# Optimization experiments

Measured on AMD Instinct MI355X. Metric: run time of the kernel, lower is better.

The kernel has to match this reference:

```python
import jax, jax.numpy as jnp
import numpy as np

ANCHORS = np.array([[10.0, 13.0], [16.0, 30.0], [33.0, 23.0]], dtype=np.float32)
NUM_ANCHORS = 3
NUM_CLASSES = 80
OBJ_SCALE = 1.0
NOOBJ_SCALE = 100.0
EPS = 1e-12


def setup_inputs() -> dict:
    key = jax.random.key(0)
    ks = jax.random.split(key, 10)
    B, A, G, C = 32, NUM_ANCHORS, 52, NUM_CLASSES
    x = jax.random.normal(ks[0], (B, A * (C + 5), G, G), dtype=jnp.float32)
    tx = jax.random.uniform(ks[1], (B, A, G, G), dtype=jnp.float32)
    ty = jax.random.uniform(ks[2], (B, A, G, G), dtype=jnp.float32)
    tw = jax.random.normal(ks[3], (B, A, G, G), dtype=jnp.float32)
    th = jax.random.normal(ks[4], (B, A, G, G), dtype=jnp.float32)
    tconf = jax.random.uniform(ks[5], (B, A, G, G), dtype=jnp.float32)
    tcls = jax.random.uniform(ks[6], (B, A, G, G, C), dtype=jnp.float32)
    sum_weights1 = jax.random.uniform(ks[7], (B, A, G, G), dtype=jnp.float32)
    obj_mask = jax.random.randint(ks[8], (B, A, G, G), 0, 2).astype(bool)
    noobj_mask = jax.random.randint(ks[9], (B, A, G, G), 0, 2).astype(bool)
    return {"x": x, "tx": tx, "ty": ty, "tw": tw, "th": th, "tconf": tconf,
            "tcls": tcls, "sum_weights1": sum_weights1, "obj_mask": obj_mask,
            "noobj_mask": noobj_mask, "img_dim": 416}


def _bce(p, t):
    # torch BCELoss(reduction='none') on already-sigmoided probs
    return -(t * jnp.log(jnp.clip(p, EPS, 1.0)) + (1.0 - t) * jnp.log(jnp.clip(1.0 - p, EPS, 1.0)))


def reference(x, tx, ty, tw, th, tconf, tcls, sum_weights1, obj_mask, noobj_mask, img_dim):
    B, _, G, _ = x.shape
    A, C = NUM_ANCHORS, NUM_CLASSES
    stride = img_dim / G  # python float
    # [B, A, G, G, C+5]
    pred = x.reshape(B, A, C + 5, G, G).transpose(0, 1, 3, 4, 2)
    px = jax.nn.sigmoid(pred[..., 0])
    py = jax.nn.sigmoid(pred[..., 1])
    pw = pred[..., 2]
    ph = pred[..., 3]
    pred_conf = jax.nn.sigmoid(pred[..., 4])
    pred_cls = jax.nn.sigmoid(pred[..., 5:])

    grid_x = jnp.arange(G, dtype=x.dtype).reshape(1, 1, 1, G)  # varies along last axis
    grid_y = jnp.arange(G, dtype=x.dtype).reshape(1, 1, G, 1)
    scaled_anchors = jnp.asarray(ANCHORS) / jnp.asarray(stride, x.dtype)
    anchor_w = scaled_anchors[:, 0].reshape(1, A, 1, 1)
    anchor_h = scaled_anchors[:, 1].reshape(1, A, 1, 1)

    sg = jax.lax.stop_gradient  # mimics .data in pred_boxes construction
    pred_boxes = jnp.stack([
        sg(px) + jnp.broadcast_to(grid_x, px.shape),
        sg(py) + jnp.broadcast_to(grid_y, py.shape),
        jnp.exp(sg(pw)) * jnp.broadcast_to(anchor_w, pw.shape),
        jnp.exp(sg(ph)) * jnp.broadcast_to(anchor_h, ph.shape),
    ], axis=-1)  # [B, A, G, G, 4]

    output = jnp.concatenate([
        pred_boxes.reshape(B, -1, 4) * stride,
        pred_conf.reshape(B, -1, 1),
        pred_cls.reshape(B, -1, C),
    ], axis=-1)

    om = obj_mask.astype(x.dtype)
    nm = noobj_mask.astype(x.dtype)
    n_obj = jnp.maximum(om.sum(), 1.0)
    n_noobj = jnp.maximum(nm.sum(), 1.0)

    def wmse(p, t):
        # mean over obj elements of mse * sum_weights1
        return jnp.sum(om * (p - t) ** 2 * sum_weights1) / n_obj

    loss_x = wmse(px, tx)
    loss_y = wmse(py, ty)
    loss_w = wmse(pw, tw)
    loss_h = wmse(ph, th)

    bce_conf = _bce(pred_conf, tconf)
    loss_conf_obj = jnp.sum(om * bce_conf * sum_weights1) / n_obj
    loss_conf_noobj = jnp.sum(nm * bce_conf) / n_noobj
    loss_conf = OBJ_SCALE * loss_conf_obj + NOOBJ_SCALE * loss_conf_noobj

    # tcls[obj_mask] yields [N, C]; mean is over N*C
    loss_cls = jnp.sum(om[..., None] * _bce(pred_cls, tcls)) / (n_obj * C)

    total_loss = loss_x + loss_y + loss_w + loss_h + loss_conf + loss_cls
    return output, total_loss
```

## Files before the change

kernel.cpp:

```cpp
#include <hip/hip_runtime.h>

#define NB 32
#define NA 3
#define GD 52
#define GG 2704
#define NC 80
#define CHN 85
#define CPW 8
#define WPP 338
#define NPLANE (NB * NA)
#define NWAVE (NPLANE * WPP)
#define WPB 4
#define NBLK (NWAVE / WPB)
#define NXQ 170
#define NTQ 160
#define LXW 680
#define AUXW 80
#define RBLK 32

__device__ __forceinline__ float sigm_u(float u) { return __builtin_amdgcn_rcpf(u); }

__global__ __launch_bounds__(256) void yolo_main(
    const float* __restrict__ x,
    const float* __restrict__ tx, const float* __restrict__ ty,
    const float* __restrict__ tw, const float* __restrict__ th,
    const float* __restrict__ tconf, const float* __restrict__ tcls,
    const float* __restrict__ sw1,
    const int* __restrict__ om, const int* __restrict__ nm,
    const int* __restrict__ imgdim,
    float* __restrict__ out,
    float4* __restrict__ partials,
    double* __restrict__ accD)
{
    __shared__ float lx_all[WPB * LXW];
    __shared__ float la_all[WPB * AUXW];

    const int tid  = threadIdx.x;
    const int widx = tid >> 6, lane = tid & 63;
    const int wid  = blockIdx.x * WPB + widx;
    const int plane = wid / WPP;
    const int sblk  = wid - plane * WPP;
    const int a = plane % NA, b = plane / NA;
    const int s0 = sblk * CPW;
    float* lx = lx_all + widx * LXW;
    float* la = la_all + widx * AUXW;

    int iv = imgdim[0];
    float imgf = (iv > 0 && iv < 65536) ? (float)iv : __int_as_float(iv);
    const float stride = imgf / (float)GD;
    const float aw = (a == 0) ? 10.0f : ((a == 1) ? 16.0f : 33.0f);
    const float ah = (a == 0) ? 13.0f : ((a == 1) ? 30.0f : 23.0f);

    const long pbase = (long)plane * GG + s0;
    const float* xb = x + ((long)b * (NA * CHN) + a * CHN) * GG + s0;
    const float* tb = tcls + pbase * NC;

    float v0 = 0.0f, v1 = 0.0f;
    if (lane < CPW) {
        float vtx = tx[pbase + lane],    vty = ty[pbase + lane];
        float vtw = tw[pbase + lane],    vth = th[pbase + lane];
        float vtc = tconf[pbase + lane], vsw = sw1[pbase + lane];
        float vom = (float)om[pbase + lane], vnm = (float)nm[pbase + lane];
        int gcell = s0 + lane;
        int gyi = gcell / GD;
        la[0 * CPW + lane] = vtx;  la[1 * CPW + lane] = vty;
        la[2 * CPW + lane] = vtw;  la[3 * CPW + lane] = vth;
        la[4 * CPW + lane] = vtc;  la[5 * CPW + lane] = vom * vsw;
        la[6 * CPW + lane] = vnm;  la[7 * CPW + lane] = vom;
        la[8 * CPW + lane] = (float)(gcell - gyi * GD);
        la[9 * CPW + lane] = (float)gyi;
        v0 = vom; v1 = vnm;
    }

    float4 xr[3];
    #pragma unroll
    for (int k = 0; k < 3; ++k) {
        int q = lane + 64 * k;
        if (q < NXQ) {
            int ch = q >> 1, sq = (q & 1) << 2;
            xr[k] = *(const float4*)(xb + (long)ch * GG + sq);
        }
    }
    __builtin_amdgcn_wave_barrier();

    float4 tr[3]; float gk[3];
    #pragma unroll
    for (int k = 0; k < 3; ++k) {
        gk[k] = 0.0f;
        int q = lane + 64 * k;
        if (q < NTQ) {
            int s = q / 20, c4 = (q - s * 20) * 4;
            float g = la[7 * CPW + s];
            gk[k] = g;
            if (g != 0.0f) tr[k] = *(const float4*)(tb + s * NC + c4);
        }
    }

    float s_obj = 0.f, s_cn = 0.f, s_cl = 0.f;

    #pragma unroll
    for (int k = 0; k < 3; ++k) {
        int q = lane + 64 * k;
        if (q >= NXQ) continue;
        int ch = q >> 1, sq = (q & 1) << 2;
        float vv[4] = { xr[k].x, xr[k].y, xr[k].z, xr[k].w };
        if (ch >= 5) {
            #pragma unroll
            for (int j = 0; j < 4; ++j)
                lx[(sq + j) * CHN + ch] = sigm_u(1.0f + __expf(-vv[j]));
        } else if (ch == 0) {
            #pragma unroll
            for (int j = 0; j < 4; ++j) {
                int s = sq + j;
                float p = sigm_u(1.0f + __expf(-vv[j]));
                float d = p - la[0 * CPW + s];
                s_obj = fmaf(la[5 * CPW + s], d * d, s_obj);
                lx[s * CHN + 0] = (p + la[8 * CPW + s]) * stride;
            }
        } else if (ch == 1) {
            #pragma unroll
            for (int j = 0; j < 4; ++j) {
                int s = sq + j;
                float p = sigm_u(1.0f + __expf(-vv[j]));
                float d = p - la[1 * CPW + s];
                s_obj = fmaf(la[5 * CPW + s], d * d, s_obj);
                lx[s * CHN + 1] = (p + la[9 * CPW + s]) * stride;
            }
        } else if (ch == 2) {
            #pragma unroll
            for (int j = 0; j < 4; ++j) {
                int s = sq + j;
                float d = vv[j] - la[2 * CPW + s];
                s_obj = fmaf(la[5 * CPW + s], d * d, s_obj);
                lx[s * CHN + 2] = __expf(vv[j]) * aw;
            }
        } else if (ch == 3) {
            #pragma unroll
            for (int j = 0; j < 4; ++j) {
                int s = sq + j;
                float d = vv[j] - la[3 * CPW + s];
                s_obj = fmaf(la[5 * CPW + s], d * d, s_obj);
                lx[s * CHN + 3] = __expf(vv[j]) * ah;
            }
        } else {
            #pragma unroll
            for (int j = 0; j < 4; ++j) {
                int s = sq + j;
                float z = vv[j];
                float u = 1.0f + __expf(-z);
                float p = sigm_u(u);
                float t = la[4 * CPW + s];
                float bb = fmaf(1.0f - t, z, __logf(u));
                s_obj = fmaf(la[5 * CPW + s], bb, s_obj);
                s_cn  = fmaf(la[6 * CPW + s], bb, s_cn);
                lx[s * CHN + 4] = p;
            }
        }
    }
    __builtin_amdgcn_wave_barrier();

    float* ob = out + pbase * CHN;
    #pragma unroll
    for (int k = 0; k < 3; ++k) {
        int q = lane + 64 * k;
        if (q < NXQ) {
            float4 w4 = *(const float4*)&lx[4 * q];
            *(float4*)(ob + 4 * q) = w4;
        }
    }

    #pragma unroll
    for (int k = 0; k < 3; ++k) {
        if (gk[k] != 0.0f) {
            int q = lane + 64 * k;
            int s = q / 20, c4 = (q - s * 20) * 4;
            int base = s * CHN + 5 + c4;
            float tt[4] = { tr[k].x, tr[k].y, tr[k].z, tr[k].w };
            #pragma unroll
            for (int j = 0; j < 4; ++j) {
                float p = lx[base + j];
                s_cl -= fmaf(tt[j], __logf(p), (1.0f - tt[j]) * __logf(1.0f - p));
            }
        }
    }
    s_obj = fmaf(s_cl, 0.0125f, s_obj);

    float v2 = s_obj, v3 = s_cn;
    #pragma unroll
    for (int off = 32; off > 0; off >>= 1) {
        v0 += __shfl_down(v0, off, 64);
        v1 += __shfl_down(v1, off, 64);
        v2 += __shfl_down(v2, off, 64);
        v3 += __shfl_down(v3, off, 64);
    }
    if (lane == 0) {
        if (partials) {
            partials[wid] = make_float4(v0, v1, v2, v3);
        } else {
            atomicAdd(&accD[0], (double)v0);
            atomicAdd(&accD[8], (double)v1);
            atomicAdd(&accD[16], (double)v2);
            atomicAdd(&accD[24], (double)v3);
        }
    }
}

__global__ __launch_bounds__(256) void yolo_reduceA(const float4* __restrict__ partials,
                                                    float4* __restrict__ stage2)
{
    __shared__ float sred[4][4];
    const int tid = threadIdx.x, wv = tid >> 6, ln = tid & 63;
    float d0 = 0, d1 = 0, d2 = 0, d3 = 0;
    for (int i = blockIdx.x * 256 + tid; i < NWAVE; i += RBLK * 256) {
        float4 p = partials[i];
        d0 += p.x; d1 += p.y; d2 += p.z; d3 += p.w;
    }
    #pragma unroll
    for (int off = 32; off > 0; off >>= 1) {
        d0 += __shfl_down(d0, off, 64);
        d1 += __shfl_down(d1, off, 64);
        d2 += __shfl_down(d2, off, 64);
        d3 += __shfl_down(d3, off, 64);
    }
    if (ln == 0) { sred[wv][0] = d0; sred[wv][1] = d1; sred[wv][2] = d2; sred[wv][3] = d3; }
    __syncthreads();
    if (tid == 0)
        stage2[blockIdx.x] = make_float4(sred[0][0] + sred[1][0] + sred[2][0] + sred[3][0],
                                         sred[0][1] + sred[1][1] + sred[2][1] + sred[3][1],
                                         sred[0][2] + sred[1][2] + sred[2][2] + sred[3][2],
                                         sred[0][3] + sred[1][3] + sred[2][3] + sred[3][3]);
}

__global__ __launch_bounds__(64) void yolo_reduceB(const float4* __restrict__ stage2,
                                                   float* __restrict__ out_loss)
{
    const int ln = threadIdx.x;
    double d0 = 0, d1 = 0, d2 = 0, d3 = 0;
    if (ln < RBLK) {
        float4 p = stage2[ln];
        d0 = p.x; d1 = p.y; d2 = p.z; d3 = p.w;
    }
    #pragma unroll
    for (int off = 32; off > 0; off >>= 1) {
        d0 += __shfl_down(d0, off, 64);
        d1 += __shfl_down(d1, off, 64);
        d2 += __shfl_down(d2, off, 64);
        d3 += __shfl_down(d3, off, 64);
    }
    if (ln == 0) {
        double nobj = fmax(d0, 1.0), nnoobj = fmax(d1, 1.0);
        *out_loss = (float)(d2 / nobj + 100.0 * d3 / nnoobj);
    }
}

__global__ void yolo_final_atomic(const double* __restrict__ accD, float* __restrict__ out_loss)
{
    double nobj = fmax(accD[0], 1.0), nnoobj = fmax(accD[8], 1.0);
    *out_loss = (float)(accD[16] / nobj + 100.0 * accD[24] / nnoobj);
}

extern "C" void kernel_launch(void* const* d_in, const int* in_sizes, int n_in,
                              void* d_out, int out_size, void* d_ws, size_t ws_size,
                              hipStream_t stream)
{
    const float* x     = (const float*)d_in[0];
    const float* tx    = (const float*)d_in[1];
    const float* ty    = (const float*)d_in[2];
    const float* tw    = (const float*)d_in[3];
    const float* th    = (const float*)d_in[4];
    const float* tconf = (const float*)d_in[5];
    const float* tcls  = (const float*)d_in[6];
    const float* sw1   = (const float*)d_in[7];
    const int*   om    = (const int*)d_in[8];
    const int*   nm    = (const int*)d_in[9];
    const int*   img   = (const int*)d_in[10];
    float* out = (float*)d_out;

    const size_t need = (size_t)(NWAVE + RBLK) * sizeof(float4);
    dim3 grid(NBLK);

    if (ws_size >= need) {
        float4* partials = (float4*)d_ws;
        float4* stage2   = partials + NWAVE;
        yolo_main<<<grid, 256, 0, stream>>>(x, tx, ty, tw, th, tconf, tcls, sw1,
                                            om, nm, img, out, partials, nullptr);
        yolo_reduceA<<<RBLK, 256, 0, stream>>>(partials, stage2);
        yolo_reduceB<<<1, 64, 0, stream>>>(stage2, out + (out_size - 1));
    } else {
        double* accD = (double*)d_ws;
        hipMemsetAsync(d_ws, 0, 32 * sizeof(double), stream);
        yolo_main<<<grid, 256, 0, stream>>>(x, tx, ty, tw, th, tconf, tcls, sw1,
                                            om, nm, img, out, nullptr, accD);
        yolo_final_atomic<<<1, 1, 0, stream>>>(accD, out + (out_size - 1));
    }
}
```

Measured before the change: 57.67 us.

## Load per-cell targets into registers across the wave and shuffle the objectness mask

Every lane now loads the eight per-cell target values (indexed by lane&7) right after the x loads are issued, instead of lanes 0-7 loading them first. The objectness flag for the tcls gating comes from a width-8 shuffle rather than shared memory, so the gated tcls loads no longer wait behind an LDS write and barrier. The class BCE is also rewritten with log2 and a single fma per element, with the -ln2/80 scale folded into one constant. The cost is redundant scalar loads across 64 lanes and a slightly reshaped auxiliary LDS layout.

```diff
diff --git a/kernel.cpp b/kernel.cpp
--- a/kernel.cpp
+++ b/kernel.cpp
@@ -15,8 +15,9 @@
 #define NXQ 170
 #define NTQ 160
 #define LXW 680
-#define AUXW 80
+#define AUXW 72
 #define RBLK 32
+#define NEG_LN2_80 (-0.008664339757f)
 
 __device__ __forceinline__ float sigm_u(float u) { return __builtin_amdgcn_rcpf(u); }
 
@@ -55,23 +56,6 @@
     const float* xb = x + ((long)b * (NA * CHN) + a * CHN) * GG + s0;
     const float* tb = tcls + pbase * NC;
 
-    float v0 = 0.0f, v1 = 0.0f;
-    if (lane < CPW) {
-        float vtx = tx[pbase + lane],    vty = ty[pbase + lane];
-        float vtw = tw[pbase + lane],    vth = th[pbase + lane];
-        float vtc = tconf[pbase + lane], vsw = sw1[pbase + lane];
-        float vom = (float)om[pbase + lane], vnm = (float)nm[pbase + lane];
-        int gcell = s0 + lane;
-        int gyi = gcell / GD;
-        la[0 * CPW + lane] = vtx;  la[1 * CPW + lane] = vty;
-        la[2 * CPW + lane] = vtw;  la[3 * CPW + lane] = vth;
-        la[4 * CPW + lane] = vtc;  la[5 * CPW + lane] = vom * vsw;
-        la[6 * CPW + lane] = vnm;  la[7 * CPW + lane] = vom;
-        la[8 * CPW + lane] = (float)(gcell - gyi * GD);
-        la[9 * CPW + lane] = (float)gyi;
-        v0 = vom; v1 = vnm;
-    }
-
     float4 xr[3];
     #pragma unroll
     for (int k = 0; k < 3; ++k) {
@@ -81,7 +65,12 @@
             xr[k] = *(const float4*)(xb + (long)ch * GG + sq);
         }
     }
-    __builtin_amdgcn_wave_barrier();
+
+    const int sc = lane & 7;
+    float r_tx = tx[pbase + sc], r_ty = ty[pbase + sc];
+    float r_tw = tw[pbase + sc], r_th = th[pbase + sc];
+    float r_tc = tconf[pbase + sc], r_sw = sw1[pbase + sc];
+    float r_om = (float)om[pbase + sc], r_nm = (float)nm[pbase + sc];
 
     float4 tr[3]; float gk[3];
     #pragma unroll
@@ -90,13 +79,25 @@
         int q = lane + 64 * k;
         if (q < NTQ) {
             int s = q / 20, c4 = (q - s * 20) * 4;
-            float g = la[7 * CPW + s];
+            float g = __shfl(r_om, s, 8);
             gk[k] = g;
             if (g != 0.0f) tr[k] = *(const float4*)(tb + s * NC + c4);
         }
     }
 
-    float s_obj = 0.f, s_cn = 0.f, s_cl = 0.f;
+    if (lane < CPW) {
+        int gcell = s0 + lane;
+        int gyi = gcell / GD;
+        la[0 * CPW + lane] = r_tx;  la[1 * CPW + lane] = r_ty;
+        la[2 * CPW + lane] = r_tw;  la[3 * CPW + lane] = r_th;
+        la[4 * CPW + lane] = r_tc;  la[5 * CPW + lane] = r_om * r_sw;
+        la[6 * CPW + lane] = r_nm;
+        la[7 * CPW + lane] = (float)(gcell - gyi * GD);
+        la[8 * CPW + lane] = (float)gyi;
+    }
+    __builtin_amdgcn_wave_barrier();
+
+    float s_obj = 0.f, s_cn = 0.f, s_cl2 = 0.f;
 
     #pragma unroll
     for (int k = 0; k < 3; ++k) {
@@ -115,7 +116,7 @@
                 float p = sigm_u(1.0f + __expf(-vv[j]));
                 float d = p - la[0 * CPW + s];
                 s_obj = fmaf(la[5 * CPW + s], d * d, s_obj);
-                lx[s * CHN + 0] = (p + la[8 * CPW + s]) * stride;
+                lx[s * CHN + 0] = (p + la[7 * CPW + s]) * stride;
             }
         } else if (ch == 1) {
             #pragma unroll
@@ -124,7 +125,7 @@
                 float p = sigm_u(1.0f + __expf(-vv[j]));
                 float d = p - la[1 * CPW + s];
                 s_obj = fmaf(la[5 * CPW + s], d * d, s_obj);
-                lx[s * CHN + 1] = (p + la[9 * CPW + s]) * stride;
+                lx[s * CHN + 1] = (p + la[8 * CPW + s]) * stride;
             }
         } else if (ch == 2) {
             #pragma unroll
@@ -178,13 +179,17 @@
             float tt[4] = { tr[k].x, tr[k].y, tr[k].z, tr[k].w };
             #pragma unroll
             for (int j = 0; j < 4; ++j) {
-                float p = lx[base + j];
-                s_cl -= fmaf(tt[j], __logf(p), (1.0f - tt[j]) * __logf(1.0f - p));
-            }
-        }
-    }
-    s_obj = fmaf(s_cl, 0.0125f, s_obj);
-
+                float p  = lx[base + j];
+                float l0 = __log2f(p);
+                float l1 = __log2f(1.0f - p);
+                s_cl2 += fmaf(tt[j], l0 - l1, l1);
+            }
+        }
+    }
+    s_obj = fmaf(s_cl2, NEG_LN2_80, s_obj);
+
+    float v0 = (lane < CPW) ? r_om : 0.0f;
+    float v1 = (lane < CPW) ? r_nm : 0.0f;
     float v2 = s_obj, v3 = s_cn;
     #pragma unroll
     for (int off = 32; off > 0; off >>= 1) {
```

New measurement: 54.73 us. 1.05x faster.
